# Performance work log

Hardware: AMD Instinct MI355X
Metric: run time of the kernel (lower is better)

## Reference

```python
import jax, jax.numpy as jnp
import numpy as np

B, T, C = 4, 2048, 2048
H, KV, D = 16, 4, 128          # head_dim = C // H
G = H // KV                     # query heads per kv head
ROPE_BASE = 10000.0


def _rope_tables(T, D, dtype):
    inv_freq = 1.0 / (ROPE_BASE ** (jnp.arange(0, D, 2, dtype=jnp.float32) / D))
    t = jnp.arange(T, dtype=jnp.float32)
    freqs = jnp.outer(t, inv_freq)                 # [T, D/2]
    emb = jnp.concatenate([freqs, freqs], axis=-1) # [T, D]
    return jnp.cos(emb).astype(dtype), jnp.sin(emb).astype(dtype)


def _rotate_half(x):
    x1, x2 = x[..., : x.shape[-1] // 2], x[..., x.shape[-1] // 2 :]
    return jnp.concatenate([-x2, x1], axis=-1)


def setup_inputs() -> dict:
    key = jax.random.key(0)
    ks = jax.random.split(key, 5)
    s = 0.02
    return {
        "x":  jax.random.normal(ks[0], (B, T, C), dtype=jnp.float32),
        "Wq": jax.random.normal(ks[1], (C, H * D), dtype=jnp.float32) * s,
        "Wk": jax.random.normal(ks[2], (C, KV * D), dtype=jnp.float32) * s,
        "Wv": jax.random.normal(ks[3], (C, KV * D), dtype=jnp.float32) * s,
        "Wo": jax.random.normal(ks[4], (C, C), dtype=jnp.float32) * s,
    }


def reference(x, Wq, Wk, Wv, Wo):
    Bc, Tc, Cc = x.shape
    q = (x @ Wq).reshape(Bc, Tc, H, D).transpose(0, 2, 1, 3)   # [B,H,T,D]
    k = (x @ Wk).reshape(Bc, Tc, KV, D).transpose(0, 2, 1, 3)  # [B,KV,T,D]
    v = (x @ Wv).reshape(Bc, Tc, KV, D).transpose(0, 2, 1, 3)  # [B,KV,T,D]

    cos, sin = _rope_tables(Tc, D, x.dtype)                    # [T,D]
    q = q * cos + _rotate_half(q) * sin
    k = k * cos + _rotate_half(k) * sin

    # GQA: broadcast KV heads instead of materializing repeat_interleave.
    # repeat_interleave over head dim == view q as [B,KV,G,T,D] sharing kv head.
    qg = q.reshape(Bc, KV, G, Tc, D)
    scale = D ** -0.5
    scores = jnp.einsum("bkgtd,bksd->bkgts", qg, k) * scale    # [B,KV,G,T,T]
    causal = jnp.tril(jnp.ones((Tc, Tc), dtype=bool))
    scores = jnp.where(causal, scores, jnp.finfo(scores.dtype).min)
    att = jax.nn.softmax(scores, axis=-1)
    out = jnp.einsum("bkgts,bksd->bkgtd", att, v)              # [B,KV,G,T,D]
    out = out.reshape(Bc, H, Tc, D).transpose(0, 2, 1, 3).reshape(Bc, Tc, Cc)
    return out @ Wo
```

## Files before the change

kernel.cpp:

```cpp
#include <hip/hip_runtime.h>
#include <cstdint>

#define DEV __device__ __forceinline__

typedef __attribute__((ext_vector_type(4))) float f32x4;
typedef __attribute__((ext_vector_type(4))) float float4v;
typedef __attribute__((ext_vector_type(8))) short bf16x8;
typedef __attribute__((ext_vector_type(4))) unsigned short ushort4v;
typedef __attribute__((ext_vector_type(2))) unsigned int uint2v;
typedef unsigned short u16;

static constexpr int Bb = 4, Tt = 2048, Hh = 16, KVh = 4, Dd = 128;
static constexpr int NQKV = 3072;

DEV u16 f2bf(float x) {
    union { float f; unsigned u; } v; v.f = x;
    unsigned r = v.u + 0x7FFF + ((v.u >> 16) & 1);
    return (u16)(r >> 16);
}
DEV float bf2f(u16 b) {
    union { unsigned u; float f; } v; v.u = ((unsigned)b) << 16;
    return v.f;
}
DEV unsigned cvtpk(float lo, float hi) {
    unsigned d;
    asm("v_cvt_pk_bf16_f32 %0, %1, %2" : "=v"(d) : "v"(lo), "v"(hi));
    return d;
}

typedef const void __attribute__((address_space(1)))* gas1;
typedef void __attribute__((address_space(3)))* las3;
DEV void gload16(const void* g, void* l) {
    __builtin_amdgcn_global_load_lds((gas1)g, (las3)l, 16, 0, 0);
}

__global__ __launch_bounds__(256) void cast_k(const float* __restrict__ x, u16* __restrict__ xb, long n4) {
    long id = (long)blockIdx.x * 256 + threadIdx.x;
    if (id >= n4) return;
    float4v v = *(const float4v*)&x[id * 4];
    ushort4v o;
    o[0] = f2bf(v[0]); o[1] = f2bf(v[1]); o[2] = f2bf(v[2]); o[3] = f2bf(v[3]);
    *(ushort4v*)&xb[id * 4] = o;
}

__global__ __launch_bounds__(256) void twt_k(const float* __restrict__ W, u16* __restrict__ Wt, int K, int N) {
    __shared__ float tile[32][33];
    int tx = threadIdx.x, ty = threadIdx.y;
    long n0 = (long)blockIdx.x * 32, k0 = (long)blockIdx.y * 32;
#pragma unroll
    for (int j = 0; j < 4; j++)
        tile[ty + j * 8][tx] = W[(k0 + ty + j * 8) * (long)N + n0 + tx];
    __syncthreads();
#pragma unroll
    for (int j = 0; j < 4; j++)
        Wt[(n0 + ty + j * 8) * (long)K + k0 + tx] = f2bf(tile[tx][ty + j * 8]);
}

__global__ __launch_bounds__(256) void tv_k(const u16* __restrict__ qkv, u16* __restrict__ vt) {
    __shared__ u16 tile[32][33];
    int tx = threadIdx.x, ty = threadIdx.y;
    int d0 = blockIdx.x * 32;
    int t0 = blockIdx.y * 32;
    int bk = blockIdx.z;
    int b = bk >> 2, kv = bk & 3;
#pragma unroll
    for (int j = 0; j < 4; j++)
        tile[ty + j * 8][tx] = qkv[(long)(b * Tt + t0 + ty + j * 8) * NQKV + 2560 + kv * Dd + d0 + tx];
    __syncthreads();
#pragma unroll
    for (int j = 0; j < 4; j++)
        vt[((long)(b * KVh + kv) * Dd + d0 + ty + j * 8) * Tt + t0 + tx] = tile[tx][ty + j * 8];
}

__global__ __launch_bounds__(256) void tables_k(float* __restrict__ cosb, float* __restrict__ sinb) {
    int id = blockIdx.x * 256 + threadIdx.x;
    int t = id >> 6, i = id & 63;
    float inv = powf(10000.0f, -(float)i * (1.0f / 64.0f));
    float f = (float)t * inv;
    cosb[id] = cosf(f);
    sinb[id] = sinf(f);
}

__global__ __launch_bounds__(256) void rope_k(u16* __restrict__ p, const float* __restrict__ cosb,
                                              const float* __restrict__ sinb, int nh, float scale, int total,
                                              long rowstride, int colbase) {
    int id = blockIdx.x * 256 + threadIdx.x;
    if (id >= total) return;
    int i = id & 63;
    int bth = id >> 6;
    int row = bth / nh;
    int t = row % Tt;
    u16* ptr = p + (long)row * rowstride + colbase + (bth % nh) * Dd;
    float x1 = bf2f(ptr[i]), x2 = bf2f(ptr[i + 64]);
    float c = cosb[t * 64 + i], s = sinb[t * 64 + i];
    ptr[i] = f2bf((x1 * c - x2 * s) * scale);
    ptr[i + 64] = f2bf((x2 * c + x1 * s) * scale);
}

template <int F32OUT>
__global__ __launch_bounds__(256) void gemm_k(const u16* __restrict__ A, const u16* __restrict__ Bt,
                                              void* __restrict__ Cout, int M, int N, int K) {
    __shared__ u16 lds[3][8192];
    const int tid = threadIdx.x;
    const int lane = tid & 63;
    const int wid = __builtin_amdgcn_readfirstlane(tid >> 6);
    const long m0 = (long)blockIdx.x * 128;
    const long n0 = (long)blockIdx.y * 128;
    const int wr = wid >> 1, wc = wid & 1;
    const int r0 = wid * 32;
    const int lrow = lane >> 2;
    const int lkb = (lane & 3) * 8;
    const u16* gA = A + (m0 + r0 + lrow) * (long)K + lkb;
    const u16* gB = Bt + (n0 + r0 + lrow) * (long)K + lkb;
    f32x4 acc[4][4] = {};
    const int fr = lane & 15, fk = (lane >> 4) * 8;
    const int NT = K >> 5;

    auto stage = [&](int t) {
        u16* lA = &lds[t % 3][r0 * 32];
        u16* lB = &lds[t % 3][4096 + r0 * 32];
        const long ko = (long)t * 32;
        gload16(gA + ko, lA);
        gload16(gA + ko + 16 * (long)K, lA + 16 * 32);
        gload16(gB + ko, lB);
        gload16(gB + ko + 16 * (long)K, lB + 16 * 32);
    };

    stage(0);
    if (NT > 1) {
        stage(1);
        asm volatile("s_waitcnt vmcnt(4)" ::: "memory");
    } else {
        asm volatile("s_waitcnt vmcnt(0)" ::: "memory");
    }
    __builtin_amdgcn_s_barrier();

    for (int kt = 0; kt < NT; ++kt) {
        if (kt + 2 < NT) stage(kt + 2);
        const u16* bufA = &lds[kt % 3][0];
        const u16* bufB = &lds[kt % 3][4096];
        bf16x8 af[4], bfr[4];
#pragma unroll
        for (int i = 0; i < 4; i++) {
            af[i] = *(const bf16x8*)&bufA[(wr * 64 + i * 16 + fr) * 32 + fk];
            bfr[i] = *(const bf16x8*)&bufB[(wc * 64 + i * 16 + fr) * 32 + fk];
        }
        __builtin_amdgcn_s_setprio(1);
#pragma unroll
        for (int i = 0; i < 4; i++)
#pragma unroll
            for (int j = 0; j < 4; j++)
                acc[i][j] = __builtin_amdgcn_mfma_f32_16x16x32_bf16(af[i], bfr[j], acc[i][j], 0, 0, 0);
        __builtin_amdgcn_s_setprio(0);
        if (kt + 2 < NT)
            asm volatile("s_waitcnt vmcnt(4)" ::: "memory");
        else if (kt + 1 < NT)
            asm volatile("s_waitcnt vmcnt(0)" ::: "memory");
        __builtin_amdgcn_s_barrier();
    }
    const int orow = (lane >> 4) * 4, ocol = lane & 15;
#pragma unroll
    for (int i = 0; i < 4; i++)
#pragma unroll
        for (int j = 0; j < 4; j++) {
            long r = m0 + wr * 64 + i * 16 + orow;
            long c = n0 + wc * 64 + j * 16 + ocol;
#pragma unroll
            for (int t = 0; t < 4; t++) {
                if (F32OUT)
                    ((float*)Cout)[(r + t) * N + c] = acc[i][j][t];
                else
                    ((u16*)Cout)[(r + t) * N + c] = f2bf(acc[i][j][t]);
            }
        }
}

__global__ __launch_bounds__(256, 2) void attn_k(const u16* __restrict__ qkv,
                                                 const u16* __restrict__ vt, u16* __restrict__ o) {
    __shared__ u16 kl[2][2][4096];
    __shared__ u16 vl[2][2][4096];
    __shared__ u16 pT[4][16][36];
    const int tid = threadIdx.x;
    const int lane = tid & 63;
    const int w = tid >> 6;
    const int kv = blockIdx.y, b = blockIdx.z;
    const int h = kv * 4 + w;
    const int fr = lane & 15, kg = lane >> 4;
    const long HD = (long)Hh * Dd;
    const long QS = (long)NQKV;
    const long kbase = (long)b * Tt * QS + 2048 + (long)kv * Dd;
    const long vbase = ((long)(b * KVh + kv)) * (long)Dd * Tt;

    auto stage = [&](int bb, int it) {
        const int s0 = it * 64;
        const int lh = lane >> 4;
#pragma unroll
        for (int s = 0; s < 2; s++) {
#pragma unroll
            for (int j = 0; j < 2; j++) {
                int c = j * 4 + w;
                int row = c * 4 + lh;
                int c16 = (lane & 15) ^ (row & 7);
                gload16(qkv + kbase + (long)(s0 + s * 32 + row) * QS + c16 * 8, &kl[bb][s][c * 512]);
            }
#pragma unroll
            for (int j = 0; j < 2; j++) {
                int c = j * 4 + w;
                int rowp = c * 4 + lh;
                int c16u = (lane & 15) ^ (rowp & 7);
                int r = rowp * 4 + (c16u >> 2);
                gload16(vt + vbase + (long)r * Tt + s0 + s * 32 + (c16u & 3) * 8, &vl[bb][s][c * 512]);
            }
        }
    };

    for (int pass = 0; pass < 2; ++pass) {
        const int qt = pass ? (int)blockIdx.x : 63 - (int)blockIdx.x;
        const int q0 = qt * 32;
        const long qbase = (long)(b * Tt + q0) * QS + (long)h * Dd;
        const long obase = (long)(b * Tt + q0) * HD + (long)h * Dd;

        bf16x8 qa[2][4];
#pragma unroll
        for (int qi = 0; qi < 2; qi++)
#pragma unroll
            for (int kc = 0; kc < 4; kc++)
                qa[qi][kc] = *(const bf16x8*)&qkv[qbase + (long)(qi * 16 + fr) * QS + kc * 32 + kg * 8];

        f32x4 ot[8][2] = {};
        float mr0 = -1e30f, mr1 = -1e30f, lr0 = 0.0f, lr1 = 0.0f;
        const int nt = (qt + 2) >> 1;

        stage(0, 0);
        __syncthreads();
        int cur = 0;
        for (int it = 0; it < nt; ++it) {
            if (it + 1 < nt) stage(cur ^ 1, it + 1);
            const int s0 = it * 64;
            f32x4 st[4][2] = {};
            __builtin_amdgcn_s_setprio(1);
#pragma unroll
            for (int kf = 0; kf < 4; kf++) {
                const int s = kf >> 1;
                const int rr = (kf & 1) * 16 + fr;
                bf16x8 ka[4];
#pragma unroll
                for (int kc = 0; kc < 4; kc++)
                    ka[kc] = *(const bf16x8*)&kl[cur][s][rr * 128 + (((kc * 4 + kg) ^ (rr & 7)) * 8)];
#pragma unroll
                for (int kc = 0; kc < 4; kc++) {
                    st[kf][0] = __builtin_amdgcn_mfma_f32_16x16x32_bf16(ka[kc], qa[0][kc], st[kf][0], 0, 0, 0);
                    st[kf][1] = __builtin_amdgcn_mfma_f32_16x16x32_bf16(ka[kc], qa[1][kc], st[kf][1], 0, 0, 0);
                }
            }
            __builtin_amdgcn_s_setprio(0);
            if (it == nt - 1) {
#pragma unroll
                for (int kf = 0; kf < 4; kf++)
#pragma unroll
                    for (int qi = 0; qi < 2; qi++) {
                        const int qq = q0 + qi * 16 + fr;
                        const int kb0 = s0 + kf * 16 + kg * 4;
#pragma unroll
                        for (int r = 0; r < 4; r++)
                            if (kb0 + r > qq) st[kf][qi][r] = -1e30f;
                    }
            }
            float tm0 = st[0][0][0], tm1 = st[0][1][0];
#pragma unroll
            for (int kf = 0; kf < 4; kf++)
#pragma unroll
                for (int r = 0; r < 4; r++)
                    if (kf | r) {
                        tm0 = fmaxf(tm0, st[kf][0][r]);
                        tm1 = fmaxf(tm1, st[kf][1][r]);
                    }
            tm0 = fmaxf(tm0, __shfl_xor(tm0, 16)); tm0 = fmaxf(tm0, __shfl_xor(tm0, 32));
            tm1 = fmaxf(tm1, __shfl_xor(tm1, 16)); tm1 = fmaxf(tm1, __shfl_xor(tm1, 32));
            if (__any(fmaxf(tm0 - mr0, tm1 - mr1) > 8.0f)) {
                float mn0 = fmaxf(mr0, tm0), mn1 = fmaxf(mr1, tm1);
                float al0 = __builtin_amdgcn_exp2f(mr0 - mn0);
                float al1 = __builtin_amdgcn_exp2f(mr1 - mn1);
                mr0 = mn0; mr1 = mn1;
                lr0 *= al0; lr1 *= al1;
#pragma unroll
                for (int df = 0; df < 8; df++) { ot[df][0] *= al0; ot[df][1] *= al1; }
            }
            float rs0 = 0.0f, rs1 = 0.0f;
#pragma unroll
            for (int kf = 0; kf < 4; kf++)
#pragma unroll
                for (int r = 0; r < 4; r++) {
                    st[kf][0][r] = __builtin_amdgcn_exp2f(st[kf][0][r] - mr0); rs0 += st[kf][0][r];
                    st[kf][1][r] = __builtin_amdgcn_exp2f(st[kf][1][r] - mr1); rs1 += st[kf][1][r];
                }
            rs0 += __shfl_xor(rs0, 16); rs0 += __shfl_xor(rs0, 32);
            rs1 += __shfl_xor(rs1, 16); rs1 += __shfl_xor(rs1, 32);
            lr0 += rs0; lr1 += rs1;
#pragma unroll
            for (int qi = 0; qi < 2; qi++)
#pragma unroll
                for (int s = 0; s < 2; s++) {
                    uint2v w0;
                    w0[0] = cvtpk(st[2 * s][qi][0], st[2 * s][qi][1]);
                    w0[1] = cvtpk(st[2 * s][qi][2], st[2 * s][qi][3]);
                    *(uint2v*)&pT[w][fr][kg * 4] = w0;
                    uint2v w1;
                    w1[0] = cvtpk(st[2 * s + 1][qi][0], st[2 * s + 1][qi][1]);
                    w1[1] = cvtpk(st[2 * s + 1][qi][2], st[2 * s + 1][qi][3]);
                    *(uint2v*)&pT[w][fr][16 + kg * 4] = w1;
                    bf16x8 bq = *(const bf16x8*)&pT[w][fr][kg * 8];
                    __builtin_amdgcn_s_setprio(1);
#pragma unroll
                    for (int df = 0; df < 8; df++) {
                        const int r = df * 16 + fr;
                        const int rowp = r >> 2;
                        const int c16 = (((r & 3) * 4 + kg) ^ (rowp & 7));
                        bf16x8 va = *(const bf16x8*)&vl[cur][s][rowp * 128 + c16 * 8];
                        ot[df][qi] = __builtin_amdgcn_mfma_f32_16x16x32_bf16(va, bq, ot[df][qi], 0, 0, 0);
                    }
                    __builtin_amdgcn_s_setprio(0);
                }
            __syncthreads();
            cur ^= 1;
        }
        const float il0 = 1.0f / lr0, il1 = 1.0f / lr1;
#pragma unroll
        for (int df = 0; df < 8; df++) {
            uint2v w0, w1;
            w0[0] = cvtpk(ot[df][0][0] * il0, ot[df][0][1] * il0);
            w0[1] = cvtpk(ot[df][0][2] * il0, ot[df][0][3] * il0);
            w1[0] = cvtpk(ot[df][1][0] * il1, ot[df][1][1] * il1);
            w1[1] = cvtpk(ot[df][1][2] * il1, ot[df][1][3] * il1);
            *(uint2v*)&o[obase + (long)(fr) * HD + df * 16 + kg * 4] = w0;
            *(uint2v*)&o[obase + (long)(16 + fr) * HD + df * 16 + kg * 4] = w1;
        }
    }
}

extern "C" void kernel_launch(void* const* d_in, const int* in_sizes, int n_in,
                              void* d_out, int out_size, void* d_ws, size_t ws_size,
                              hipStream_t stream) {
    (void)in_sizes; (void)n_in; (void)out_size; (void)ws_size;
    const float* x = (const float*)d_in[0];
    const float* Wq = (const float*)d_in[1];
    const float* Wk = (const float*)d_in[2];
    const float* Wv = (const float*)d_in[3];
    const float* Wo = (const float*)d_in[4];

    char* ws = (char*)d_ws;
    u16* xb   = (u16*)(ws + 0);
    u16* vtb  = (u16*)(ws + 50331648);
    u16* wqt  = (u16*)(ws + 58720256);
    u16* wkt  = (u16*)(ws + 67108864);
    u16* wvt  = (u16*)(ws + 69206016);
    u16* wot  = (u16*)(ws + 71303168);
    float* cosb = (float*)(ws + 79691776);
    float* sinb = (float*)(ws + 80216064);
    u16* qkv = (u16*)d_out;

    dim3 tb(32, 8);
    cast_k<<<16384, 256, 0, stream>>>(x, xb, 4194304);
    twt_k<<<dim3(64, 64), tb, 0, stream>>>(Wq, wqt, 2048, 2048);
    twt_k<<<dim3(16, 64), tb, 0, stream>>>(Wk, wkt, 2048, 512);
    twt_k<<<dim3(16, 64), tb, 0, stream>>>(Wv, wvt, 2048, 512);
    twt_k<<<dim3(64, 64), tb, 0, stream>>>(Wo, wot, 2048, 2048);
    tables_k<<<512, 256, 0, stream>>>(cosb, sinb);

    gemm_k<0><<<dim3(64, 24), 256, 0, stream>>>(xb, wqt, qkv, 8192, NQKV, 2048);

    rope_k<<<32768, 256, 0, stream>>>(qkv, cosb, sinb, 16, 0.1275174316f, 8388608, NQKV, 0);
    rope_k<<<8192, 256, 0, stream>>>(qkv, cosb, sinb, 4, 1.0f, 2097152, NQKV, 2048);
    tv_k<<<dim3(4, 64, 16), tb, 0, stream>>>(qkv, vtb);

    attn_k<<<dim3(32, 4, 4), 256, 0, stream>>>(qkv, vtb, xb);

    gemm_k<1><<<dim3(64, 16), 256, 0, stream>>>(xb, wot, d_out, 8192, 2048, 2048);
}
```

Before: 372.9 us.

## Enlarge GEMM tiles to 256x128x64 with 8 waves and XOR-swizzled LDS

```diff
diff --git a/kernel.cpp b/kernel.cpp
--- a/kernel.cpp
+++ b/kernel.cpp
@@ -98,73 +98,84 @@
 }
 
 template <int F32OUT>
-__global__ __launch_bounds__(256) void gemm_k(const u16* __restrict__ A, const u16* __restrict__ Bt,
+__global__ __launch_bounds__(512) void gemm_k(const u16* __restrict__ A, const u16* __restrict__ Bt,
                                               void* __restrict__ Cout, int M, int N, int K) {
-    __shared__ u16 lds[3][8192];
+    __shared__ u16 lds[3][24576];
     const int tid = threadIdx.x;
     const int lane = tid & 63;
-    const int wid = __builtin_amdgcn_readfirstlane(tid >> 6);
-    const long m0 = (long)blockIdx.x * 128;
+    const int w = __builtin_amdgcn_readfirstlane(tid >> 6);
+    const int wm = w >> 1, wn = w & 1;
+    const long m0 = (long)blockIdx.x * 256;
     const long n0 = (long)blockIdx.y * 128;
-    const int wr = wid >> 1, wc = wid & 1;
-    const int r0 = wid * 32;
-    const int lrow = lane >> 2;
-    const int lkb = (lane & 3) * 8;
-    const u16* gA = A + (m0 + r0 + lrow) * (long)K + lkb;
-    const u16* gB = Bt + (n0 + r0 + lrow) * (long)K + lkb;
+    const int NT = K >> 6;
+    const int l8 = lane >> 3, s8 = lane & 7;
+    const int fr = lane & 15, kg = lane >> 4;
+
+    auto stage = [&](int t) {
+        u16* base = lds[t % 3];
+        const long ko = (long)t * 64;
+#pragma unroll
+        for (int c4 = 0; c4 < 4; c4++) {
+            int c = w * 4 + c4;
+            int row = c * 8 + l8;
+            int slog = s8 ^ (l8 & 7);
+            gload16(A + (m0 + row) * (long)K + ko + slog * 8, base + c * 512);
+        }
+#pragma unroll
+        for (int c2 = 0; c2 < 2; c2++) {
+            int c = w * 2 + c2;
+            int row = c * 8 + l8;
+            int slog = s8 ^ (l8 & 7);
+            gload16(Bt + (n0 + row) * (long)K + ko + slog * 8, base + 16384 + c * 512);
+        }
+    };
+
     f32x4 acc[4][4] = {};
-    const int fr = lane & 15, fk = (lane >> 4) * 8;
-    const int NT = K >> 5;
-
-    auto stage = [&](int t) {
-        u16* lA = &lds[t % 3][r0 * 32];
-        u16* lB = &lds[t % 3][4096 + r0 * 32];
-        const long ko = (long)t * 32;
-        gload16(gA + ko, lA);
-        gload16(gA + ko + 16 * (long)K, lA + 16 * 32);
-        gload16(gB + ko, lB);
-        gload16(gB + ko + 16 * (long)K, lB + 16 * 32);
-    };
-
     stage(0);
     if (NT > 1) {
         stage(1);
-        asm volatile("s_waitcnt vmcnt(4)" ::: "memory");
+        asm volatile("s_waitcnt vmcnt(6)" ::: "memory");
     } else {
         asm volatile("s_waitcnt vmcnt(0)" ::: "memory");
     }
     __builtin_amdgcn_s_barrier();
 
-    for (int kt = 0; kt < NT; ++kt) {
-        if (kt + 2 < NT) stage(kt + 2);
-        const u16* bufA = &lds[kt % 3][0];
-        const u16* bufB = &lds[kt % 3][4096];
-        bf16x8 af[4], bfr[4];
-#pragma unroll
-        for (int i = 0; i < 4; i++) {
-            af[i] = *(const bf16x8*)&bufA[(wr * 64 + i * 16 + fr) * 32 + fk];
-            bfr[i] = *(const bf16x8*)&bufB[(wc * 64 + i * 16 + fr) * 32 + fk];
-        }
-        __builtin_amdgcn_s_setprio(1);
-#pragma unroll
-        for (int i = 0; i < 4; i++)
-#pragma unroll
-            for (int j = 0; j < 4; j++)
-                acc[i][j] = __builtin_amdgcn_mfma_f32_16x16x32_bf16(af[i], bfr[j], acc[i][j], 0, 0, 0);
-        __builtin_amdgcn_s_setprio(0);
-        if (kt + 2 < NT)
-            asm volatile("s_waitcnt vmcnt(4)" ::: "memory");
-        else if (kt + 1 < NT)
+    for (int t = 0; t < NT; ++t) {
+        if (t + 2 < NT) stage(t + 2);
+        const u16* sa = lds[t % 3];
+        const u16* sb = sa + 16384;
+#pragma unroll
+        for (int ks = 0; ks < 2; ks++) {
+            bf16x8 af[4], bfr[4];
+#pragma unroll
+            for (int i = 0; i < 4; i++) {
+                const int row = wm * 64 + i * 16 + fr;
+                af[i] = *(const bf16x8*)&sa[row * 64 + (((ks * 4 + kg) ^ (row & 7)) * 8)];
+                const int col = wn * 64 + i * 16 + fr;
+                bfr[i] = *(const bf16x8*)&sb[col * 64 + (((ks * 4 + kg) ^ (col & 7)) * 8)];
+            }
+            __builtin_amdgcn_s_setprio(1);
+#pragma unroll
+            for (int i = 0; i < 4; i++)
+#pragma unroll
+                for (int j = 0; j < 4; j++)
+                    acc[i][j] = __builtin_amdgcn_mfma_f32_16x16x32_bf16(af[i], bfr[j], acc[i][j], 0, 0, 0);
+            __builtin_amdgcn_s_setprio(0);
+        }
+        if (t + 2 < NT)
+            asm volatile("s_waitcnt vmcnt(6)" ::: "memory");
+        else if (t + 1 < NT)
             asm volatile("s_waitcnt vmcnt(0)" ::: "memory");
         __builtin_amdgcn_s_barrier();
     }
+
     const int orow = (lane >> 4) * 4, ocol = lane & 15;
 #pragma unroll
     for (int i = 0; i < 4; i++)
 #pragma unroll
         for (int j = 0; j < 4; j++) {
-            long r = m0 + wr * 64 + i * 16 + orow;
-            long c = n0 + wc * 64 + j * 16 + ocol;
+            long r = m0 + wm * 64 + i * 16 + orow;
+            long c = n0 + wn * 64 + j * 16 + ocol;
 #pragma unroll
             for (int t = 0; t < 4; t++) {
                 if (F32OUT)
@@ -367,7 +378,7 @@
     twt_k<<<dim3(64, 64), tb, 0, stream>>>(Wo, wot, 2048, 2048);
     tables_k<<<512, 256, 0, stream>>>(cosb, sinb);
 
-    gemm_k<0><<<dim3(64, 24), 256, 0, stream>>>(xb, wqt, qkv, 8192, NQKV, 2048);
+    gemm_k<0><<<dim3(32, 24), 512, 0, stream>>>(xb, wqt, qkv, 8192, NQKV, 2048);
 
     rope_k<<<32768, 256, 0, stream>>>(qkv, cosb, sinb, 16, 0.1275174316f, 8388608, NQKV, 0);
     rope_k<<<8192, 256, 0, stream>>>(qkv, cosb, sinb, 4, 1.0f, 2097152, NQKV, 2048);
@@ -375,5 +386,5 @@
 
     attn_k<<<dim3(32, 4, 4), 256, 0, stream>>>(qkv, vtb, xb);
 
-    gemm_k<1><<<dim3(64, 16), 256, 0, stream>>>(xb, wot, d_out, 8192, 2048, 2048);
-}
+    gemm_k<1><<<dim3(32, 16), 512, 0, stream>>>(xb, wot, d_out, 8192, 2048, 2048);
+}
```

After: 364.8 us. -2.2%, faster.
